# Kernel tuning notes

Measured on AMD Instinct MI355X. Metric: run time of the kernel, lower is better.

Reference implementation:

```python
import jax, jax.numpy as jnp
import numpy as np

DIM = 192
HEADS = 6
WS = 12       # window_size
STRIDE = 3    # dilation stride for mask


def build_mask():
    # Static (ws*ws, ws*ws) additive mask: only neighbors with dh%stride==0 and
    # dw%stride==0 are allowed, self (0,0) excluded.
    coords = np.stack(np.meshgrid(np.arange(WS), np.arange(WS), indexing='ij'))
    coords = coords.reshape(2, -1)                       # (2, ws*ws)
    rel = coords[:, :, None] - coords[:, None, :]        # (2, N, N)
    valid = (rel[0] % STRIDE == 0) & (rel[1] % STRIDE == 0)
    valid &= ~((rel[0] == 0) & (rel[1] == 0))
    mask = np.where(valid, 0.0, -np.inf).astype(np.float32)
    return jnp.asarray(mask)


def setup_inputs() -> dict:
    key = jax.random.key(0)
    k1, k2, k3 = jax.random.split(key, 3)
    x = jax.random.normal(k1, (4, DIM, 256, 256), dtype=jnp.float32)
    w_qkv = jax.random.normal(k2, (3 * DIM, DIM), dtype=jnp.float32) * 0.02
    w_proj = jax.random.normal(k3, (DIM, DIM), dtype=jnp.float32) * 0.02
    return {"x": x, "w_qkv": w_qkv, "w_proj": w_proj}


def reference(x, w_qkv, w_proj):
    B, C, H, W = x.shape
    mask = build_mask()                                   # (N, N), N = WS*WS
    pad_r = (WS - W % WS) % WS
    pad_b = (WS - H % WS) % WS
    x = jnp.pad(x, ((0, 0), (0, 0), (0, pad_b), (0, pad_r)), mode='reflect')
    Hp, Wp = x.shape[2], x.shape[3]
    nh, nw = Hp // WS, Wp // WS
    # b c h w -> b h w c -> (b nh nw, ws*ws, c)
    xw = x.transpose(0, 2, 3, 1)
    xw = xw.reshape(B, nh, WS, nw, WS, C).transpose(0, 1, 3, 2, 4, 5)
    xw = xw.reshape(B * nh * nw, WS * WS, C)
    qkv = xw @ w_qkv.T                                    # (bw, n, 3C)
    q, k, v = jnp.split(qkv, 3, axis=-1)
    d = C // HEADS
    scale = d ** (-0.5)
    def heads(t):
        return t.reshape(t.shape[0], t.shape[1], HEADS, d).transpose(0, 2, 1, 3)
    q, k, v = heads(q), heads(k), heads(v)                # (bw, h, n, d)
    attn = jnp.einsum('whnd,whmd->whnm', q * scale, k)
    attn = attn + mask[None, None]
    attn = jax.nn.softmax(attn, axis=-1)
    out = jnp.einsum('whnm,whmd->whnd', attn, v)
    out = out.transpose(0, 2, 1, 3).reshape(out.shape[0], WS * WS, C)
    out = out @ w_proj.T
    # merge windows: (b nh nw, ws*ws, c) -> b c Hp Wp
    out = out.reshape(B, nh, nw, WS, WS, C).transpose(0, 1, 3, 2, 4, 5)
    out = out.reshape(B, Hp, Wp, C).transpose(0, 3, 1, 2)
    return out[:, :, :H, :W]
```

## Files before the change

### kernel.cpp

```cpp
#include <hip/hip_runtime.h>
#include <hip/hip_bf16.h>

typedef __bf16 bf16x8 __attribute__((ext_vector_type(8)));
typedef float f32x4 __attribute__((ext_vector_type(4)));
typedef unsigned int u32x4 __attribute__((ext_vector_type(4)));

#define WSZ 12
#define NTOK 144
#define RES 256
#define NHW 22
#define NWIN (4*NHW*NHW)
#define SCALE 0.17677669529663687f
#define XS 200
#define QS 40
#define VTS 152

#define WQ_ELEMS (576*192)
#define WP_ELEMS (192*192)
#define WS_NEED ((WQ_ELEMS + WP_ELEMS) * 2)

#define OFF_Q  57600
#define OFF_K  (57600 + 2*11520)
#define OFF_VT (57600 + 4*11520)
#define SMEM_BYTES (OFF_VT + 2*32*VTS*2 + 128)

static __device__ __forceinline__ unsigned f2u(float f) {
    return (unsigned)__builtin_bit_cast(unsigned short, __float2bfloat16(f));
}
static __device__ __forceinline__ unsigned pk2(float a, float b) {
    return f2u(a) | (f2u(b) << 16);
}
static __device__ __forceinline__ bf16x8 ld8(const void* p) {
    return *(const bf16x8*)p;
}
static __device__ __forceinline__ bf16x8 wfrag(const float* p) {
    const float4* p4 = (const float4*)p;
    float4 lo = p4[0], hi = p4[1];
    u32x4 u = { pk2(lo.x, lo.y), pk2(lo.z, lo.w), pk2(hi.x, hi.y), pk2(hi.z, hi.w) };
    return __builtin_bit_cast(bf16x8, u);
}

__global__ __launch_bounds__(256) void conv_w(const float* __restrict__ wq,
                                              const float* __restrict__ wp,
                                              __hip_bfloat16* __restrict__ dst) {
    int i = blockIdx.x * 256 + threadIdx.x;
    if (i < WQ_ELEMS) dst[i] = __float2bfloat16(wq[i]);
    if (i < WP_ELEMS) dst[WQ_ELEMS + i] = __float2bfloat16(wp[i]);
}

template<bool WB>
__global__ __launch_bounds__(768, 3) void wsa_kernel(
    const float* __restrict__ x,
    const float* __restrict__ w_qkv,
    const float* __restrict__ w_proj,
    const __hip_bfloat16* __restrict__ wqb,
    const __hip_bfloat16* __restrict__ wpb,
    float* __restrict__ out)
{
    __shared__ __align__(16) unsigned char smem[SMEM_BYTES];
    __hip_bfloat16 (* const xw)[XS] = reinterpret_cast<__hip_bfloat16(*)[XS]>(smem);
    float          (* const stg)[100] = reinterpret_cast<float(*)[100]>(smem);
    __hip_bfloat16* const vTp = reinterpret_cast<__hip_bfloat16*>(smem + OFF_VT);

    const int tid  = threadIdx.x;
    const int lane = tid & 63;
    const int wv   = tid >> 6;
    const int col  = lane & 15;
    const int grp  = lane >> 4;

    const int wid = blockIdx.x;
    const int b   = wid / (NHW * NHW);
    const int r0  = wid % (NHW * NHW);
    const int wh  = r0 / NHW;
    const int ww  = r0 % NHW;

    for (int u = tid; u < 24 * NTOK; u += 768) {
        int c8 = u / NTOK;
        int t  = u - c8 * NTOK;
        int ty = t / WSZ, tx = t - ty * WSZ;
        int h = wh * WSZ + ty; if (h >= RES) h = 2 * RES - 2 - h;
        int w = ww * WSZ + tx; if (w >= RES) w = 2 * RES - 2 - w;
        const float* px = x + ((size_t)(b * 192 + c8 * 8) * RES + h) * RES + w;
        u32x4 uv;
        #pragma unroll
        for (int j = 0; j < 4; ++j)
            uv[j] = pk2(px[(size_t)(2 * j) * RES * RES], px[(size_t)(2 * j + 1) * RES * RES]);
        *(u32x4*)&xw[t][c8 * 8] = uv;
    }
    __syncthreads();

    f32x4 pacc[9];
    #pragma unroll
    for (int m = 0; m < 9; ++m) pacc[m] = (f32x4){0.f, 0.f, 0.f, 0.f};

    const int mh   = wv & 1;
    const int n6   = wv >> 1;
    const int kind = n6 >> 1;
    const int h2q  = n6 & 1;
    const int mt0  = mh ? 4 : 0;
    const int nmt  = mh ? 5 : 4;

    for (int hp = 0; hp < 3; ++hp) {
        {
            const int hh    = hp * 2 + h2q;
            const int rbase = kind * 192 + hh * 32;
            f32x4 acc[2][5];
            #pragma unroll
            for (int d = 0; d < 2; ++d)
                #pragma unroll
                for (int m = 0; m < 5; ++m) acc[d][m] = (f32x4){0.f, 0.f, 0.f, 0.f};
            #pragma unroll
            for (int k0 = 0; k0 < 6; ++k0) {
                const bf16x8 B0 = WB ? ld8(wqb + (size_t)(rbase + col) * 192 + k0 * 32 + grp * 8)
                                     : wfrag(w_qkv + (size_t)(rbase + col) * 192 + k0 * 32 + grp * 8);
                const bf16x8 B1 = WB ? ld8(wqb + (size_t)(rbase + 16 + col) * 192 + k0 * 32 + grp * 8)
                                     : wfrag(w_qkv + (size_t)(rbase + 16 + col) * 192 + k0 * 32 + grp * 8);
                #pragma unroll
                for (int m = 0; m < 5; ++m) {
                    if (m < nmt) {
                        const bf16x8 Af = ld8(&xw[(mt0 + m) * 16 + col][k0 * 32 + grp * 8]);
                        acc[0][m] = __builtin_amdgcn_mfma_f32_16x16x32_bf16(Af, B0, acc[0][m], 0, 0, 0);
                        acc[1][m] = __builtin_amdgcn_mfma_f32_16x16x32_bf16(Af, B1, acc[1][m], 0, 0, 0);
                    }
                }
            }
            const float qs = (kind == 0) ? SCALE : 1.f;
            if (kind < 2) {
                __hip_bfloat16 (* const pl)[QS] = reinterpret_cast<__hip_bfloat16(*)[QS]>(
                    smem + (kind == 0 ? OFF_Q : OFF_K) + h2q * 11520);
                #pragma unroll
                for (int m = 0; m < 5; ++m) if (m < nmt) {
                    #pragma unroll
                    for (int r = 0; r < 4; ++r) {
                        const int trow = (mt0 + m) * 16 + grp * 4 + r;
                        pl[trow][col]      = __float2bfloat16(acc[0][m][r] * qs);
                        pl[trow][16 + col] = __float2bfloat16(acc[1][m][r] * qs);
                    }
                }
            } else {
                #pragma unroll
                for (int m = 0; m < 5; ++m) if (m < nmt) {
                    #pragma unroll
                    for (int r = 0; r < 4; ++r) {
                        const int t  = (mt0 + m) * 16 + grp * 4 + r;
                        const int ti = t / WSZ, tj = t - ti * WSZ;
                        const int cs   = (ti % 3) * 3 + (tj % 3);
                        const int ctok = (ti / 3) * 4 + (tj / 3);
                        vTp[(size_t)(h2q * 32 + col) * VTS + cs * 16 + ctok]      = __float2bfloat16(acc[0][m][r]);
                        vTp[(size_t)(h2q * 32 + 16 + col) * VTS + cs * 16 + ctok] = __float2bfloat16(acc[1][m][r]);
                    }
                }
            }
        }
        __syncthreads();

        for (int u = wv; u < 18; u += 12) {
            const int h2 = u / 9;
            const int cs = u % 9;
            __hip_bfloat16 (* const qPl)[QS] = reinterpret_cast<__hip_bfloat16(*)[QS]>(smem + OFF_Q + h2 * 11520);
            __hip_bfloat16 (* const kPl)[QS] = reinterpret_cast<__hip_bfloat16(*)[QS]>(smem + OFF_K + h2 * 11520);
            const int ci = cs / 3, cj = cs % 3;
            const int tcol = (ci + 3 * (col >> 2)) * WSZ + cj + 3 * (col & 3);
            const bf16x8 Kf = ld8(&kPl[tcol][grp * 8]);
            const bf16x8 Qf = ld8(&qPl[tcol][grp * 8]);
            f32x4 S = {0.f, 0.f, 0.f, 0.f};
            S = __builtin_amdgcn_mfma_f32_16x16x32_bf16(Kf, Qf, S, 0, 0, 0);
            float e[4]; float mx = -1e30f;
            #pragma unroll
            for (int r = 0; r < 4; ++r) {
                float s = (grp * 4 + r == col) ? -1e30f : S[r];
                e[r] = s;
                mx = fmaxf(mx, s);
            }
            mx = fmaxf(mx, __shfl_xor(mx, 16));
            mx = fmaxf(mx, __shfl_xor(mx, 32));
            float sum = 0.f;
            #pragma unroll
            for (int r = 0; r < 4; ++r) { e[r] = __expf(e[r] - mx); sum += e[r]; }
            sum += __shfl_xor(sum, 16);
            sum += __shfl_xor(sum, 32);
            const float inv = 1.f / sum;
            const unsigned w0 = pk2(e[0] * inv, e[1] * inv);
            const unsigned w1 = pk2(e[2] * inv, e[3] * inv);
            u32x4 pa = {0u, 0u, 0u, 0u};
            {
                const int sA = (col + 32 * grp) * 4;
                int q0 = __builtin_amdgcn_ds_bpermute(sA,      (int)w0);
                int q1 = __builtin_amdgcn_ds_bpermute(sA,      (int)w1);
                int q2 = __builtin_amdgcn_ds_bpermute(sA + 64, (int)w0);
                int q3 = __builtin_amdgcn_ds_bpermute(sA + 64, (int)w1);
                if (grp < 2) pa = (u32x4){(unsigned)q0, (unsigned)q1, (unsigned)q2, (unsigned)q3};
            }
            const bf16x8 PB = __builtin_bit_cast(bf16x8, pa);
            #pragma unroll
            for (int d0 = 0; d0 < 2; ++d0) {
                const bf16x8 VA = ld8(&vTp[(size_t)(h2 * 32 + d0 * 16 + col) * VTS + cs * 16 + (grp & 1) * 8]);
                f32x4 O = {0.f, 0.f, 0.f, 0.f};
                O = __builtin_amdgcn_mfma_f32_16x16x32_bf16(VA, PB, O, 0, 0, 0);
                #pragma unroll
                for (int r = 0; r < 4; ++r)
                    qPl[tcol][d0 * 16 + grp * 4 + r] = __float2bfloat16(O[r]);
            }
        }
        __syncthreads();

        {
            #pragma unroll
            for (int h2 = 0; h2 < 2; ++h2) {
                const int hh = hp * 2 + h2;
                const bf16x8 Bf = WB ? ld8(wpb + (size_t)(wv * 16 + col) * 192 + hh * 32 + grp * 8)
                                     : wfrag(w_proj + (size_t)(wv * 16 + col) * 192 + hh * 32 + grp * 8);
                __hip_bfloat16 (* const aoPl)[QS] = reinterpret_cast<__hip_bfloat16(*)[QS]>(smem + OFF_Q + h2 * 11520);
                #pragma unroll
                for (int mt = 0; mt < 9; ++mt) {
                    const bf16x8 Af = ld8(&aoPl[mt * 16 + col][grp * 8]);
                    pacc[mt] = __builtin_amdgcn_mfma_f32_16x16x32_bf16(Af, Bf, pacc[mt], 0, 0, 0);
                }
            }
        }
        __syncthreads();
    }

    for (int half = 0; half < 2; ++half) {
        if (half) __syncthreads();
        if (wv >= half * 6 && wv < half * 6 + 6) {
            const int ocl = (wv - half * 6) * 16 + col;
            #pragma unroll
            for (int mt = 0; mt < 9; ++mt)
                #pragma unroll
                for (int r = 0; r < 4; ++r)
                    stg[mt * 16 + grp * 4 + r][ocl] = pacc[mt][r];
        }
        __syncthreads();
        const int txo = tid % 12;
        const int u0  = tid / 12;
        for (int it = 0; it < 18; ++it) {
            int u = u0 + it * 64;
            int oc_l = u / 12, ty = u % 12;
            int h = wh * WSZ + ty, w = ww * WSZ + txo;
            if (h < RES && w < RES)
                out[((size_t)(b * 192 + half * 96 + oc_l) * RES + h) * RES + w] = stg[ty * WSZ + txo][oc_l];
        }
    }
}

extern "C" void kernel_launch(void* const* d_in, const int* in_sizes, int n_in,
                              void* d_out, int out_size, void* d_ws, size_t ws_size,
                              hipStream_t stream) {
    const float* x      = (const float*)d_in[0];
    const float* w_qkv  = (const float*)d_in[1];
    const float* w_proj = (const float*)d_in[2];
    float* out = (float*)d_out;
    if (ws_size >= (size_t)WS_NEED) {
        __hip_bfloat16* wqb = (__hip_bfloat16*)d_ws;
        __hip_bfloat16* wpb = wqb + WQ_ELEMS;
        conv_w<<<dim3((WQ_ELEMS + 255) / 256), dim3(256), 0, stream>>>(w_qkv, w_proj, wqb);
        wsa_kernel<true><<<dim3(NWIN), dim3(768), 0, stream>>>(x, w_qkv, w_proj, wqb, wpb, out);
    } else {
        wsa_kernel<false><<<dim3(NWIN), dim3(768), 0, stream>>>(x, w_qkv, w_proj, nullptr, nullptr, out);
    }
}
```

Before: 339.5 us.

## Overlap output projection with next head-pair QKV, vectorize epilogue stores

```diff
diff --git a/kernel.cpp b/kernel.cpp
--- a/kernel.cpp
+++ b/kernel.cpp
@@ -14,15 +14,17 @@
 #define XS 200
 #define QS 40
 #define VTS 152
+#define STS 148
 
 #define WQ_ELEMS (576*192)
 #define WP_ELEMS (192*192)
 #define WS_NEED ((WQ_ELEMS + WP_ELEMS) * 2)
 
 #define OFF_Q  57600
-#define OFF_K  (57600 + 2*11520)
-#define OFF_VT (57600 + 4*11520)
-#define SMEM_BYTES (OFF_VT + 2*32*VTS*2 + 128)
+#define OFF_K  (OFF_Q + 2*11520)
+#define OFF_VT (OFF_K + 2*11520)
+#define OFF_AO (OFF_VT + 2*32*VTS*2)
+#define SMEM_BYTES (OFF_AO + 2*NTOK*QS*2)
 
 static __device__ __forceinline__ unsigned f2u(float f) {
     return (unsigned)__builtin_bit_cast(unsigned short, __float2bfloat16(f));
@@ -58,8 +60,8 @@
     float* __restrict__ out)
 {
     __shared__ __align__(16) unsigned char smem[SMEM_BYTES];
-    __hip_bfloat16 (* const xw)[XS] = reinterpret_cast<__hip_bfloat16(*)[XS]>(smem);
-    float          (* const stg)[100] = reinterpret_cast<float(*)[100]>(smem);
+    __hip_bfloat16 (* const xw)[XS]  = reinterpret_cast<__hip_bfloat16(*)[XS]>(smem);
+    float          (* const stg)[STS] = reinterpret_cast<float(*)[STS]>(smem);
     __hip_bfloat16* const vTp = reinterpret_cast<__hip_bfloat16*>(smem + OFF_VT);
 
     const int tid  = threadIdx.x;
@@ -68,11 +70,12 @@
     const int col  = lane & 15;
     const int grp  = lane >> 4;
 
-    const int wid = blockIdx.x;
-    const int b   = wid / (NHW * NHW);
-    const int r0  = wid % (NHW * NHW);
-    const int wh  = r0 / NHW;
-    const int ww  = r0 % NHW;
+    const int wid0 = blockIdx.x;
+    const int wid  = (wid0 & 7) * (NWIN / 8) + (wid0 >> 3);
+    const int b    = wid / (NHW * NHW);
+    const int r0   = wid % (NHW * NHW);
+    const int wh   = r0 / NHW;
+    const int ww   = r0 % NHW;
 
     for (int u = tid; u < 24 * NTOK; u += 768) {
         int c8 = u / NTOK;
@@ -100,6 +103,22 @@
     const int mt0  = mh ? 4 : 0;
     const int nmt  = mh ? 5 : 4;
 
+    auto do_proj = [&](int hpp) {
+        #pragma unroll
+        for (int h2 = 0; h2 < 2; ++h2) {
+            const int hh = hpp * 2 + h2;
+            const bf16x8 Bf = WB ? ld8(wpb + (size_t)(wv * 16 + col) * 192 + hh * 32 + grp * 8)
+                                 : wfrag(w_proj + (size_t)(wv * 16 + col) * 192 + hh * 32 + grp * 8);
+            const __hip_bfloat16 (* const aoPl)[QS] =
+                reinterpret_cast<const __hip_bfloat16(*)[QS]>(smem + OFF_AO + h2 * 11520);
+            #pragma unroll
+            for (int mt = 0; mt < 9; ++mt) {
+                const bf16x8 Af = ld8(&aoPl[mt * 16 + col][grp * 8]);
+                pacc[mt] = __builtin_amdgcn_mfma_f32_16x16x32_bf16(Af, Bf, pacc[mt], 0, 0, 0);
+            }
+        }
+    };
+
     for (int hp = 0; hp < 3; ++hp) {
         {
             const int hh    = hp * 2 + h2q;
@@ -151,6 +170,7 @@
                     }
                 }
             }
+            if (hp > 0) do_proj(hp - 1);
         }
         __syncthreads();
 
@@ -159,6 +179,7 @@
             const int cs = u % 9;
             __hip_bfloat16 (* const qPl)[QS] = reinterpret_cast<__hip_bfloat16(*)[QS]>(smem + OFF_Q + h2 * 11520);
             __hip_bfloat16 (* const kPl)[QS] = reinterpret_cast<__hip_bfloat16(*)[QS]>(smem + OFF_K + h2 * 11520);
+            __hip_bfloat16 (* const aoPl)[QS] = reinterpret_cast<__hip_bfloat16(*)[QS]>(smem + OFF_AO + h2 * 11520);
             const int ci = cs / 3, cj = cs % 3;
             const int tcol = (ci + 3 * (col >> 2)) * WSZ + cj + 3 * (col & 3);
             const bf16x8 Kf = ld8(&kPl[tcol][grp * 8]);
@@ -199,47 +220,36 @@
                 O = __builtin_amdgcn_mfma_f32_16x16x32_bf16(VA, PB, O, 0, 0, 0);
                 #pragma unroll
                 for (int r = 0; r < 4; ++r)
-                    qPl[tcol][d0 * 16 + grp * 4 + r] = __float2bfloat16(O[r]);
+                    aoPl[tcol][d0 * 16 + grp * 4 + r] = __float2bfloat16(O[r]);
             }
         }
         __syncthreads();
-
-        {
-            #pragma unroll
-            for (int h2 = 0; h2 < 2; ++h2) {
-                const int hh = hp * 2 + h2;
-                const bf16x8 Bf = WB ? ld8(wpb + (size_t)(wv * 16 + col) * 192 + hh * 32 + grp * 8)
-                                     : wfrag(w_proj + (size_t)(wv * 16 + col) * 192 + hh * 32 + grp * 8);
-                __hip_bfloat16 (* const aoPl)[QS] = reinterpret_cast<__hip_bfloat16(*)[QS]>(smem + OFF_Q + h2 * 11520);
-                #pragma unroll
-                for (int mt = 0; mt < 9; ++mt) {
-                    const bf16x8 Af = ld8(&aoPl[mt * 16 + col][grp * 8]);
-                    pacc[mt] = __builtin_amdgcn_mfma_f32_16x16x32_bf16(Af, Bf, pacc[mt], 0, 0, 0);
-                }
-            }
-        }
-        __syncthreads();
-    }
-
-    for (int half = 0; half < 2; ++half) {
-        if (half) __syncthreads();
-        if (wv >= half * 6 && wv < half * 6 + 6) {
-            const int ocl = (wv - half * 6) * 16 + col;
-            #pragma unroll
-            for (int mt = 0; mt < 9; ++mt)
-                #pragma unroll
-                for (int r = 0; r < 4; ++r)
-                    stg[mt * 16 + grp * 4 + r][ocl] = pacc[mt][r];
-        }
-        __syncthreads();
-        const int txo = tid % 12;
-        const int u0  = tid / 12;
-        for (int it = 0; it < 18; ++it) {
-            int u = u0 + it * 64;
-            int oc_l = u / 12, ty = u % 12;
-            int h = wh * WSZ + ty, w = ww * WSZ + txo;
-            if (h < RES && w < RES)
-                out[((size_t)(b * 192 + half * 96 + oc_l) * RES + h) * RES + w] = stg[ty * WSZ + txo][oc_l];
+    }
+
+    do_proj(2);
+    __syncthreads();
+
+    {
+        const int ocl = wv * 16 + col;
+        #pragma unroll
+        for (int mt = 0; mt < 9; ++mt) {
+            float4 v4 = make_float4(pacc[mt][0], pacc[mt][1], pacc[mt][2], pacc[mt][3]);
+            *(float4*)&stg[ocl][mt * 16 + grp * 4] = v4;
+        }
+    }
+    __syncthreads();
+    #pragma unroll
+    for (int it = 0; it < 9; ++it) {
+        int v = tid + it * 768;
+        int seg = v % 3;
+        int rest = v / 3;
+        int ty = rest % 12;
+        int oc = rest / 12;
+        int h  = wh * WSZ + ty;
+        int w0 = ww * WSZ + seg * 4;
+        if (h < RES && w0 < RES) {
+            float4 val = *(const float4*)&stg[oc][ty * 12 + seg * 4];
+            *(float4*)&out[((size_t)(b * 192 + oc) * RES + h) * RES + w0] = val;
         }
     }
 }
```

Result: faster. 292.9 us, median of 2 (-13.7%).
